# Optimization experiments

Hardware: AMD Instinct MI355X
Metric: run time of the kernel (lower is better)

Reference implementation:

```python
import jax, jax.numpy as jnp
import numpy as np

NUM_BASES = 8
DEGREE = 3
KSIZE = 3
DOMAIN = (0.0, 1.0)


def bspline_basis(x, degree, knots):
    """Cox-de Boor recursion, vectorized over all elements of x.
    x: [...] float; knots: [num_bases + degree + 1].
    Returns basis values of shape [..., num_bases].
    (The original torch code evaluates this same recursion per-tap inside
    nested loops; here it is evaluated once, batched, with correct knot
    index bookkeeping. Uniform distinct knots -> no zero denominators.)
    """
    xe = x[..., None]  # [..., 1]
    # degree-0: indicator of each knot interval -> [..., L-1]
    B = ((knots[:-1] <= xe) & (xe < knots[1:])).astype(x.dtype)
    for d in range(1, degree + 1):
        left = (xe - knots[:-(d + 1)]) / (knots[d:-1] - knots[:-(d + 1)]) * B[..., :-1]
        right = (knots[d + 1:] - xe) / (knots[d + 1:] - knots[1:-d]) * B[..., 1:]
        B = left + right  # [..., L-d-1]
    return B  # [..., num_bases]


def setup_inputs() -> dict:
    key = jax.random.key(0)
    k1, k2 = jax.random.split(key)
    # inputs uniform in [0,1) so they lie inside the B-spline domain
    x = jax.random.uniform(k1, (16, 64, 64, 64), dtype=jnp.float32)
    # per-tap spline coefficients: [Cout, Cin, K, K, num_bases]
    coeff = jax.random.normal(k2, (64, 64, KSIZE, KSIZE, NUM_BASES), dtype=jnp.float32)
    return {"x": x, "coeff": coeff}


def reference(x, coeff):
    # normalize to domain (identity for domain=(0,1), kept for faithfulness)
    xn = (x - DOMAIN[0]) / (DOMAIN[1] - DOMAIN[0])
    knots = jnp.linspace(DOMAIN[0], DOMAIN[1], NUM_BASES + DEGREE + 1, dtype=x.dtype)
    # spline basis for every input element: [B, Cin, H, W, nb]
    phi = bspline_basis(xn, DEGREE, knots)
    Bn, Cin, H, W, nb = phi.shape
    Cout = coeff.shape[0]
    # The KAN conv  out[b,o,h,w] = sum_{j,k,l,m} phi[b,j,h+k,w+l,m]*coeff[o,j,k,l,m]
    # is exactly a VALID conv with Cin*nb input channels.
    phi_c = jnp.transpose(phi, (0, 1, 4, 2, 3)).reshape(Bn, Cin * nb, H, W)
    w = jnp.transpose(coeff, (0, 1, 4, 2, 3)).reshape(Cout, Cin * nb, KSIZE, KSIZE)
    out = jax.lax.conv_general_dilated(
        phi_c, w, window_strides=(1, 1), padding="VALID",
        dimension_numbers=("NCHW", "OIHW", "NCHW"))
    return out  # [B, Cout, H-K+1, W-K+1]
```

## Files before the change

kernel.cpp:

```cpp
#include <hip/hip_runtime.h>
#include <hip/hip_bf16.h>


typedef short v8s __attribute__((ext_vector_type(8)));
typedef float v4f __attribute__((ext_vector_type(4)));
typedef unsigned long long u64;
typedef u64 v2u64 __attribute__((ext_vector_type(2)));

#define B_N   16
#define CIN   64
#define COUT  64
#define H_IN  64
#define W_IN  64
#define NB    8
#define HO    62
#define WO    62
#define JC    8
#define NCH   (CIN / JC)
#define ELEMS (3 * JC * W_IN)
#define EPT   (ELEMS / 256)

__device__ __forceinline__ ushort f2bf(float f) {
    uint xu = __float_as_uint(f);
    return (ushort)((xu + 0x7fffu + ((xu >> 16) & 1u)) >> 16);
}

__global__ void prep_coeff_kernel(const float* __restrict__ coeff, ushort* __restrict__ bt) {
    int n = blockIdx.x * 256 + threadIdx.x;
    if (n >= 576 * COUT * NB) return;
    int m = n & 7;
    int o = (n >> 3) & 63;
    int t = n >> 9;
    int j = t / 9;
    int r9 = t - j * 9;
    float v = coeff[(((o * CIN + j) * 9 + r9) << 3) + m];
    bt[n] = f2bf(v);
}

template<bool USE_BT>
__global__ __launch_bounds__(256, 4) void kan_conv_kernel(
        const float* __restrict__ x, const ushort* __restrict__ cb,
        const float* __restrict__ coeff_f, float* __restrict__ out) {
    const int h    = blockIdx.x;
    const int b    = blockIdx.y;
    const int tid  = threadIdx.x;
    const int lane = tid & 63;
    const int wv   = tid >> 6;
    const int g    = lane >> 4;
    const int l15  = lane & 15;
    const int obase = (wv >> 1) << 5;
    const int wbase = (wv & 1) << 5;

    __shared__ __align__(16) ushort phi_lds[3 * JC * W_IN * NB];
    __shared__ uint lut[72];

    if (tid < 72) {
        int tap = tid;
        int j  = tap / 9;
        int r9 = tap - j * 9;
        int kt = r9 / 3;
        int lt = r9 - kt * 3;
        lut[tap] = (uint)(((kt * JC + j) * W_IN) * NB) | ((uint)lt << 16)
                 | ((uint)j << 20) | ((uint)r9 << 24);
    }

    v4f acc00 = {0.f, 0.f, 0.f, 0.f};
    v4f acc01 = acc00, acc10 = acc00, acc11 = acc00;
    const int aoff = obase + l15;

    float xv[EPT];
    #pragma unroll
    for (int it = 0; it < EPT; ++it) {
        int n  = it * 256 + tid;
        int kt = n >> 9;
        int j  = (n >> 6) & (JC - 1);
        int w  = n & (W_IN - 1);
        xv[it] = x[((b * CIN + j) * H_IN + (h + kt)) * W_IN + w];
    }

    for (int jc = 0; jc < NCH; ++jc) {
        #pragma unroll
        for (int it = 0; it < EPT; ++it) {
            int n = it * 256 + tid;
            float s  = xv[it] * 11.0f;
            int i0 = (int)s;
            i0 = i0 < 0 ? 0 : (i0 > 10 ? 10 : i0);
            float u  = s - (float)i0;
            float um = 1.0f - u;
            float u2 = u * u, u3 = u2 * u;
            const float inv6 = 1.0f / 6.0f;
            float n0 = um * um * um * inv6;
            float n1 = (3.0f * u3 - 6.0f * u2 + 4.0f) * inv6;
            float n2 = (-3.0f * u3 + 3.0f * u2 + 3.0f * u + 1.0f) * inv6;
            float n3 = u3 * inv6;
            u64 V = (u64)f2bf(n0) | ((u64)f2bf(n1) << 16)
                  | ((u64)f2bf(n2) << 32) | ((u64)f2bf(n3) << 48);
            int bi = i0 - 3;
            u64 lo = bi < 0 ? (V >> (uint)(-16 * bi))
                   : bi < 4 ? (V << (uint)(16 * bi)) : 0ull;
            u64 hi = bi <= 0 ? 0ull
                   : bi < 4 ? (V >> (uint)(64 - 16 * bi))
                   : (V << (uint)(16 * bi - 64));
            v2u64 pk; pk[0] = lo; pk[1] = hi;
            *reinterpret_cast<v2u64*>(&phi_lds[n << 3]) = pk;
        }
        if (jc + 1 < NCH) {
            int j0n = (jc + 1) * JC;
            #pragma unroll
            for (int it = 0; it < EPT; ++it) {
                int n  = it * 256 + tid;
                int kt = n >> 9;
                int j  = (n >> 6) & (JC - 1);
                int w  = n & (W_IN - 1);
                xv[it] = x[((b * CIN + j0n + j) * H_IN + (h + kt)) * W_IN + w];
            }
        }
        __syncthreads();
        const int t0 = jc * JC * 9;
        const v8s* cbv = USE_BT ? reinterpret_cast<const v8s*>(cb) : nullptr;
        #pragma unroll 6
        for (int kk = 0; kk < (JC * 9 * NB) / 32; ++kk) {
            int tap = (kk << 2) + g;
            uint e = lut[tap];
            int philoc = (int)(e & 0xffffu);
            int lt     = (int)((e >> 16) & 3u);
            int w0 = wbase + l15 + lt;
            int w1 = w0 + 16;
            w0 = w0 < 63 ? w0 : 63;
            w1 = w1 < 63 ? w1 : 63;
            v8s pb0 = *reinterpret_cast<const v8s*>(&phi_lds[philoc + (w0 << 3)]);
            v8s pb1 = *reinterpret_cast<const v8s*>(&phi_lds[philoc + (w1 << 3)]);
            v8s pa0, pa1;
            if constexpr (USE_BT) {
                const v8s* pa = cbv + ((t0 + tap) << 6) + aoff;
                pa0 = pa[0];
                pa1 = pa[16];
            } else {
                int j  = (int)((e >> 20) & 15u);
                int r9 = (int)((e >> 24) & 15u);
                const float* cf = coeff_f + (((aoff * CIN + (jc * JC + j)) * 9 + r9) << 3);
                #pragma unroll
                for (int z = 0; z < 8; ++z) pa0[z] = (short)f2bf(cf[z]);
                const float* cf2 = cf + (CIN * 9 * NB * 16);
                #pragma unroll
                for (int z = 0; z < 8; ++z) pa1[z] = (short)f2bf(cf2[z]);
            }
            acc00 = __builtin_amdgcn_mfma_f32_16x16x32_bf16(pa0, pb0, acc00, 0, 0, 0);
            acc01 = __builtin_amdgcn_mfma_f32_16x16x32_bf16(pa0, pb1, acc01, 0, 0, 0);
            acc10 = __builtin_amdgcn_mfma_f32_16x16x32_bf16(pa1, pb0, acc10, 0, 0, 0);
            acc11 = __builtin_amdgcn_mfma_f32_16x16x32_bf16(pa1, pb1, acc11, 0, 0, 0);
        }
        __syncthreads();
    }

    const int wc0 = wbase + l15;
    const int wc1 = wc0 + 16;
    #pragma unroll
    for (int i = 0; i < 2; ++i) {
        v4f a0 = (i == 0) ? acc00 : acc10;
        v4f a1 = (i == 0) ? acc01 : acc11;
        int o = obase + i * 16 + (g << 2);
        #pragma unroll
        for (int r = 0; r < 4; ++r) {
            int off = ((b * COUT + o + r) * HO + h) * WO;
            if (wc0 < WO) out[off + wc0] = a0[r];
            if (wc1 < WO) out[off + wc1] = a1[r];
        }
    }
}

extern "C" void kernel_launch(void* const* d_in, const int* in_sizes, int n_in,
                              void* d_out, int out_size, void* d_ws, size_t ws_size,
                              hipStream_t stream) {
    const float* x     = (const float*)d_in[0];
    const float* coeff = (const float*)d_in[1];
    float* out = (float*)d_out;

    const size_t bt_bytes = (size_t)576 * COUT * NB * 2;
    bool use_bt = ws_size >= bt_bytes;

    if (use_bt) {
        ushort* bt = (ushort*)d_ws;
        prep_coeff_kernel<<<(576 * COUT * NB + 255) / 256, 256, 0, stream>>>(coeff, bt);
        kan_conv_kernel<true><<<dim3(HO, B_N), 256, 0, stream>>>(x, bt, coeff, out);
    } else {
        kan_conv_kernel<false><<<dim3(HO, B_N), 256, 0, stream>>>(x, nullptr, coeff, out);
    }
}
```

Baseline: 59.32 us.

## Compute two output rows per block and reuse coefficient fragments across rows

Each block now produces two adjacent output rows from four loaded input rows instead of one row from three. Every coefficient fragment loaded for kernel row r feeds both output rows, so weight traffic per output falls and input rows are shared across the pair. Each wave now covers all 64 output channels for a 16-wide column strip. The phi LDS layout is padded with a row stride of 520 to ease bank conflicts. The cost is more accumulator registers, a drop in launch bounds occupancy from 4 to 2 blocks, and half as many blocks in the grid.

After: 75.69 us. 27.6% more time.

```diff
diff --git a/kernel.cpp b/kernel.cpp
--- a/kernel.cpp
+++ b/kernel.cpp
@@ -17,7 +17,10 @@
 #define WO    62
 #define JC    8
 #define NCH   (CIN / JC)
-#define ELEMS (3 * JC * W_IN)
+#define NROWS 4
+#define ROWSTRIDE 520
+#define RSTRIDE   (JC * ROWSTRIDE)
+#define ELEMS (NROWS * JC * W_IN)
 #define EPT   (ELEMS / 256)
 
 __device__ __forceinline__ ushort f2bf(float f) {
@@ -38,50 +41,56 @@
 }
 
 template<bool USE_BT>
-__global__ __launch_bounds__(256, 4) void kan_conv_kernel(
+__global__ __launch_bounds__(256, 2) void kan_conv_kernel(
         const float* __restrict__ x, const ushort* __restrict__ cb,
         const float* __restrict__ coeff_f, float* __restrict__ out) {
-    const int h    = blockIdx.x;
+    const int h0   = blockIdx.x * 2;
     const int b    = blockIdx.y;
     const int tid  = threadIdx.x;
     const int lane = tid & 63;
-    const int wv   = tid >> 6;
+    const int wq   = tid >> 6;
     const int g    = lane >> 4;
     const int l15  = lane & 15;
-    const int obase = (wv >> 1) << 5;
-    const int wbase = (wv & 1) << 5;
 
-    __shared__ __align__(16) ushort phi_lds[3 * JC * W_IN * NB];
-    __shared__ uint lut[72];
+    __shared__ __align__(16) ushort phi_lds[NROWS * RSTRIDE];
 
-    if (tid < 72) {
-        int tap = tid;
-        int j  = tap / 9;
-        int r9 = tap - j * 9;
-        int kt = r9 / 3;
-        int lt = r9 - kt * 3;
-        lut[tap] = (uint)(((kt * JC + j) * W_IN) * NB) | ((uint)lt << 16)
-                 | ((uint)j << 20) | ((uint)r9 << 24);
+    int baddr[6];
+    int abase[6];
+    #pragma unroll
+    for (int s = 0; s < 6; ++s) {
+        int c   = s * 4 + g;
+        int jl  = c / 3;
+        int lc  = c - jl * 3;
+        int bq  = wq * 16 + l15 + lc;
+        bq = bq < 63 ? bq : 63;
+        baddr[s] = (jl * ROWSTRIDE + bq * NB) * 2;
+        abase[s] = ((jl * 9 + lc) * COUT + l15) * 16;
     }
 
-    v4f acc00 = {0.f, 0.f, 0.f, 0.f};
-    v4f acc01 = acc00, acc10 = acc00, acc11 = acc00;
-    const int aoff = obase + l15;
+    v4f acc0[4], acc1[4];
+    #pragma unroll
+    for (int ot = 0; ot < 4; ++ot) {
+        acc0[ot] = (v4f){0.f, 0.f, 0.f, 0.f};
+        acc1[ot] = (v4f){0.f, 0.f, 0.f, 0.f};
+    }
 
     float xv[EPT];
     #pragma unroll
     for (int it = 0; it < EPT; ++it) {
-        int n  = it * 256 + tid;
-        int kt = n >> 9;
-        int j  = (n >> 6) & (JC - 1);
-        int w  = n & (W_IN - 1);
-        xv[it] = x[((b * CIN + j) * H_IN + (h + kt)) * W_IN + w];
+        int n = it * 256 + tid;
+        int r = n >> 9;
+        int j = (n >> 6) & (JC - 1);
+        int w = n & (W_IN - 1);
+        xv[it] = x[((b * CIN + j) * H_IN + (h0 + r)) * W_IN + w];
     }
 
     for (int jc = 0; jc < NCH; ++jc) {
         #pragma unroll
         for (int it = 0; it < EPT; ++it) {
             int n = it * 256 + tid;
+            int r = n >> 9;
+            int j = (n >> 6) & (JC - 1);
+            int w = n & (W_IN - 1);
             float s  = xv[it] * 11.0f;
             int i0 = (int)s;
             i0 = i0 < 0 ? 0 : (i0 > 10 ? 10 : i0);
@@ -102,69 +111,70 @@
                    : bi < 4 ? (V >> (uint)(64 - 16 * bi))
                    : (V << (uint)(16 * bi - 64));
             v2u64 pk; pk[0] = lo; pk[1] = hi;
-            *reinterpret_cast<v2u64*>(&phi_lds[n << 3]) = pk;
+            *reinterpret_cast<v2u64*>(&phi_lds[(r * JC + j) * ROWSTRIDE + w * NB]) = pk;
         }
         if (jc + 1 < NCH) {
             int j0n = (jc + 1) * JC;
             #pragma unroll
             for (int it = 0; it < EPT; ++it) {
-                int n  = it * 256 + tid;
-                int kt = n >> 9;
-                int j  = (n >> 6) & (JC - 1);
-                int w  = n & (W_IN - 1);
-                xv[it] = x[((b * CIN + j0n + j) * H_IN + (h + kt)) * W_IN + w];
+                int n = it * 256 + tid;
+                int r = n >> 9;
+                int j = (n >> 6) & (JC - 1);
+                int w = n & (W_IN - 1);
+                xv[it] = x[((b * CIN + j0n + j) * H_IN + (h0 + r)) * W_IN + w];
             }
         }
         __syncthreads();
-        const int t0 = jc * JC * 9;
-        const v8s* cbv = USE_BT ? reinterpret_cast<const v8s*>(cb) : nullptr;
-        #pragma unroll 6
-        for (int kk = 0; kk < (JC * 9 * NB) / 32; ++kk) {
-            int tap = (kk << 2) + g;
-            uint e = lut[tap];
-            int philoc = (int)(e & 0xffffu);
-            int lt     = (int)((e >> 16) & 3u);
-            int w0 = wbase + l15 + lt;
-            int w1 = w0 + 16;
-            w0 = w0 < 63 ? w0 : 63;
-            w1 = w1 < 63 ? w1 : 63;
-            v8s pb0 = *reinterpret_cast<const v8s*>(&phi_lds[philoc + (w0 << 3)]);
-            v8s pb1 = *reinterpret_cast<const v8s*>(&phi_lds[philoc + (w1 << 3)]);
-            v8s pa0, pa1;
-            if constexpr (USE_BT) {
-                const v8s* pa = cbv + ((t0 + tap) << 6) + aoff;
-                pa0 = pa[0];
-                pa1 = pa[16];
-            } else {
-                int j  = (int)((e >> 20) & 15u);
-                int r9 = (int)((e >> 24) & 15u);
-                const float* cf = coeff_f + (((aoff * CIN + (jc * JC + j)) * 9 + r9) << 3);
-                #pragma unroll
-                for (int z = 0; z < 8; ++z) pa0[z] = (short)f2bf(cf[z]);
-                const float* cf2 = cf + (CIN * 9 * NB * 16);
-                #pragma unroll
-                for (int z = 0; z < 8; ++z) pa1[z] = (short)f2bf(cf2[z]);
+        const char* cbb  = (const char*)cb + (size_t)(jc * JC * 9) * (COUT * NB * 2);
+        const char* ldsb = (const char*)phi_lds;
+        const int j0 = jc * JC;
+        #pragma unroll
+        for (int s = 0; s < 6; ++s) {
+            v8s ak[3][4];
+            #pragma unroll
+            for (int r = 0; r < NROWS; ++r) {
+                v8s pb = *reinterpret_cast<const v8s*>(ldsb + baddr[s] + r * (RSTRIDE * 2));
+                if (r < 3) {
+                    #pragma unroll
+                    for (int ot = 0; ot < 4; ++ot) {
+                        if constexpr (USE_BT) {
+                            ak[r][ot] = *reinterpret_cast<const v8s*>(
+                                cbb + abase[s] + r * (3 * COUT * NB * 2) + ot * (16 * NB * 2));
+                        } else {
+                            int c  = s * 4 + g;
+                            int jl = c / 3;
+                            int lc = c - jl * 3;
+                            int o  = ot * 16 + l15;
+                            const float* cf = coeff_f +
+                                (((o * CIN + (j0 + jl)) * 9 + (r * 3 + lc)) << 3);
+                            #pragma unroll
+                            for (int z = 0; z < 8; ++z) ak[r][ot][z] = (short)f2bf(cf[z]);
+                        }
+                        acc0[ot] = __builtin_amdgcn_mfma_f32_16x16x32_bf16(ak[r][ot], pb, acc0[ot], 0, 0, 0);
+                    }
+                }
+                if (r >= 1) {
+                    #pragma unroll
+                    for (int ot = 0; ot < 4; ++ot) {
+                        acc1[ot] = __builtin_amdgcn_mfma_f32_16x16x32_bf16(ak[r - 1][ot], pb, acc1[ot], 0, 0, 0);
+                    }
+                }
             }
-            acc00 = __builtin_amdgcn_mfma_f32_16x16x32_bf16(pa0, pb0, acc00, 0, 0, 0);
-            acc01 = __builtin_amdgcn_mfma_f32_16x16x32_bf16(pa0, pb1, acc01, 0, 0, 0);
-            acc10 = __builtin_amdgcn_mfma_f32_16x16x32_bf16(pa1, pb0, acc10, 0, 0, 0);
-            acc11 = __builtin_amdgcn_mfma_f32_16x16x32_bf16(pa1, pb1, acc11, 0, 0, 0);
         }
         __syncthreads();
     }
 
-    const int wc0 = wbase + l15;
-    const int wc1 = wc0 + 16;
-    #pragma unroll
-    for (int i = 0; i < 2; ++i) {
-        v4f a0 = (i == 0) ? acc00 : acc10;
-        v4f a1 = (i == 0) ? acc01 : acc11;
-        int o = obase + i * 16 + (g << 2);
+    const int w = wq * 16 + l15;
+    if (w < WO) {
         #pragma unroll
-        for (int r = 0; r < 4; ++r) {
-            int off = ((b * COUT + o + r) * HO + h) * WO;
-            if (wc0 < WO) out[off + wc0] = a0[r];
-            if (wc1 < WO) out[off + wc1] = a1[r];
+        for (int ot = 0; ot < 4; ++ot) {
+            int o = ot * 16 + (g << 2);
+            #pragma unroll
+            for (int r = 0; r < 4; ++r) {
+                int base = ((b * COUT + o + r) * HO + h0) * WO + w;
+                out[base]      = acc0[ot][r];
+                out[base + WO] = acc1[ot][r];
+            }
         }
     }
 }
@@ -182,8 +192,8 @@
     if (use_bt) {
         ushort* bt = (ushort*)d_ws;
         prep_coeff_kernel<<<(576 * COUT * NB + 255) / 256, 256, 0, stream>>>(coeff, bt);
-        kan_conv_kernel<true><<<dim3(HO, B_N), 256, 0, stream>>>(x, bt, coeff, out);
+        kan_conv_kernel<true><<<dim3(HO / 2, B_N), 256, 0, stream>>>(x, bt, coeff, out);
     } else {
-        kan_conv_kernel<false><<<dim3(HO, B_N), 256, 0, stream>>>(x, nullptr, coeff, out);
+        kan_conv_kernel<false><<<dim3(HO / 2, B_N), 256, 0, stream>>>(x, nullptr, coeff, out);
     }
 }
```

## Compute two output rows per block with register-pipelined spline basis

Applied to the files above, without the earlier changes.

The main kernel now has each block produce two output rows. It loads four input rows of basis values into LDS and reuses each coefficient fragment across both rows, so redundant basis computation and coefficient loads per row are reduced. The basis evaluation for the next channel chunk is interleaved with the MFMA loop in registers, overlapping ALU work with matrix math. The grid is halved, the launch bound drops to 2 blocks per SM and register use rises, which lowers occupancy and parallelism.

New measurement: 69.25 us. 16.7% more time.

```diff
diff --git a/kernel.cpp b/kernel.cpp
--- a/kernel.cpp
+++ b/kernel.cpp
@@ -17,8 +17,6 @@
 #define WO    62
 #define JC    8
 #define NCH   (CIN / JC)
-#define ELEMS (3 * JC * W_IN)
-#define EPT   (ELEMS / 256)
 
 __device__ __forceinline__ ushort f2bf(float f) {
     uint xu = __float_as_uint(f);
@@ -37,10 +35,156 @@
     bt[n] = f2bf(v);
 }
 
-template<bool USE_BT>
-__global__ __launch_bounds__(256, 4) void kan_conv_kernel(
+#define MFMA(a, b, c) __builtin_amdgcn_mfma_f32_16x16x32_bf16((a), (b), (c), 0, 0, 0)
+
+__global__ __launch_bounds__(256, 2) void kan_conv_hp(
         const float* __restrict__ x, const ushort* __restrict__ cb,
-        const float* __restrict__ coeff_f, float* __restrict__ out) {
+        float* __restrict__ out) {
+    const int h0   = blockIdx.x * 2;
+    const int b    = blockIdx.y;
+    const int tid  = threadIdx.x;
+    const int lane = tid & 63;
+    const int wv   = tid >> 6;
+    const int oh   = wv >> 1;
+    const int wh   = wv & 1;
+    const int g    = lane >> 4;
+    const int l15  = lane & 15;
+
+    __shared__ __align__(16) ushort phi_lds[4 * JC * W_IN * NB];
+
+    int baddr0[6], baddr1[6], abase[6];
+    #pragma unroll
+    for (int s = 0; s < 6; ++s) {
+        int c  = s * 4 + g;
+        int jl = c / 3;
+        int lc = c - jl * 3;
+        int w0 = wh * 32 + l15 + lc;
+        int w1 = w0 + 16; w1 = w1 < 63 ? w1 : 63;
+        baddr0[s] = jl * 1024 + w0 * 16;
+        baddr1[s] = jl * 1024 + w1 * 16;
+        abase[s]  = ((jl * 9 + lc) * COUT + oh * 32 + l15) * 16;
+    }
+
+    v4f acc[2][2][2];
+    #pragma unroll
+    for (int h = 0; h < 2; ++h)
+        #pragma unroll
+        for (int ot = 0; ot < 2; ++ot)
+            #pragma unroll
+            for (int wf = 0; wf < 2; ++wf)
+                acc[h][ot][wf] = (v4f){0.f, 0.f, 0.f, 0.f};
+
+    float xreg[8];
+    v2u64 phiv[8];
+
+    auto xload = [&](int jcn) {
+        int j0n = jcn * JC;
+        #pragma unroll
+        for (int it = 0; it < 8; ++it) {
+            int n = it * 256 + tid;
+            xreg[it] = x[((b * CIN + j0n + ((n >> 6) & 7)) * H_IN
+                          + (h0 + (n >> 9))) * W_IN + (n & 63)];
+        }
+    };
+    auto phiE = [&](int e) {
+        float s_ = xreg[e] * 11.0f;
+        int i0 = (int)s_;
+        i0 = i0 < 0 ? 0 : (i0 > 10 ? 10 : i0);
+        float u  = s_ - (float)i0;
+        float um = 1.0f - u;
+        float u2 = u * u, u3 = u2 * u;
+        const float inv6 = 1.0f / 6.0f;
+        float n0 = um * um * um * inv6;
+        float n1 = (3.0f * u3 - 6.0f * u2 + 4.0f) * inv6;
+        float n2 = (-3.0f * u3 + 3.0f * u2 + 3.0f * u + 1.0f) * inv6;
+        float n3 = u3 * inv6;
+        u64 V = (u64)f2bf(n0) | ((u64)f2bf(n1) << 16)
+              | ((u64)f2bf(n2) << 32) | ((u64)f2bf(n3) << 48);
+        int bi = i0 - 3;
+        u64 lo = bi < 0 ? (V >> (uint)(-16 * bi))
+               : bi < 4 ? (V << (uint)(16 * bi)) : 0ull;
+        u64 hi = bi <= 0 ? 0ull
+               : bi < 4 ? (V >> (uint)(64 - 16 * bi))
+               : (V << (uint)(16 * bi - 64));
+        phiv[e][0] = lo; phiv[e][1] = hi;
+    };
+
+    xload(0);
+    #pragma unroll
+    for (int e = 0; e < 8; ++e) phiE(e);
+
+    for (int jc = 0; jc < NCH; ++jc) {
+        __syncthreads();
+        #pragma unroll
+        for (int it = 0; it < 8; ++it)
+            *reinterpret_cast<v2u64*>(&phi_lds[(it * 256 + tid) << 3]) = phiv[it];
+        if (jc + 1 < NCH) xload(jc + 1);
+        __syncthreads();
+        const char* bb  = (const char*)phi_lds;
+        const char* cbb = (const char*)cb + (size_t)jc * (72 * COUT * NB * 2);
+        #pragma unroll
+        for (int s = 0; s < 6; ++s) {
+            v8s pb0 = *reinterpret_cast<const v8s*>(bb + baddr0[s]);
+            v8s pb1 = *reinterpret_cast<const v8s*>(bb + baddr1[s]);
+            v8s a00 = *reinterpret_cast<const v8s*>(cbb + abase[s]);
+            v8s a01 = *reinterpret_cast<const v8s*>(cbb + abase[s] + 256);
+            acc[0][0][0] = MFMA(a00, pb0, acc[0][0][0]);
+            acc[0][0][1] = MFMA(a00, pb1, acc[0][0][1]);
+            acc[0][1][0] = MFMA(a01, pb0, acc[0][1][0]);
+            acc[0][1][1] = MFMA(a01, pb1, acc[0][1][1]);
+            pb0 = *reinterpret_cast<const v8s*>(bb + 8192 + baddr0[s]);
+            pb1 = *reinterpret_cast<const v8s*>(bb + 8192 + baddr1[s]);
+            v8s a10 = *reinterpret_cast<const v8s*>(cbb + abase[s] + 3072);
+            v8s a11 = *reinterpret_cast<const v8s*>(cbb + abase[s] + 3072 + 256);
+            acc[0][0][0] = MFMA(a10, pb0, acc[0][0][0]);
+            acc[0][0][1] = MFMA(a10, pb1, acc[0][0][1]);
+            acc[0][1][0] = MFMA(a11, pb0, acc[0][1][0]);
+            acc[0][1][1] = MFMA(a11, pb1, acc[0][1][1]);
+            acc[1][0][0] = MFMA(a00, pb0, acc[1][0][0]);
+            acc[1][0][1] = MFMA(a00, pb1, acc[1][0][1]);
+            acc[1][1][0] = MFMA(a01, pb0, acc[1][1][0]);
+            acc[1][1][1] = MFMA(a01, pb1, acc[1][1][1]);
+            pb0 = *reinterpret_cast<const v8s*>(bb + 16384 + baddr0[s]);
+            pb1 = *reinterpret_cast<const v8s*>(bb + 16384 + baddr1[s]);
+            v8s a20 = *reinterpret_cast<const v8s*>(cbb + abase[s] + 6144);
+            v8s a21 = *reinterpret_cast<const v8s*>(cbb + abase[s] + 6144 + 256);
+            acc[0][0][0] = MFMA(a20, pb0, acc[0][0][0]);
+            acc[0][0][1] = MFMA(a20, pb1, acc[0][0][1]);
+            acc[0][1][0] = MFMA(a21, pb0, acc[0][1][0]);
+            acc[0][1][1] = MFMA(a21, pb1, acc[0][1][1]);
+            acc[1][0][0] = MFMA(a10, pb0, acc[1][0][0]);
+            acc[1][0][1] = MFMA(a10, pb1, acc[1][0][1]);
+            acc[1][1][0] = MFMA(a11, pb0, acc[1][1][0]);
+            acc[1][1][1] = MFMA(a11, pb1, acc[1][1][1]);
+            pb0 = *reinterpret_cast<const v8s*>(bb + 24576 + baddr0[s]);
+            pb1 = *reinterpret_cast<const v8s*>(bb + 24576 + baddr1[s]);
+            acc[1][0][0] = MFMA(a20, pb0, acc[1][0][0]);
+            acc[1][0][1] = MFMA(a20, pb1, acc[1][0][1]);
+            acc[1][1][0] = MFMA(a21, pb0, acc[1][1][0]);
+            acc[1][1][1] = MFMA(a21, pb1, acc[1][1][1]);
+            if (s < 4 && jc + 1 < NCH) { phiE(2 * s); phiE(2 * s + 1); }
+        }
+    }
+
+    const int w0c = wh * 32 + l15;
+    const int w1c = w0c + 16;
+    #pragma unroll
+    for (int h = 0; h < 2; ++h)
+        #pragma unroll
+        for (int ot = 0; ot < 2; ++ot) {
+            int o = oh * 32 + ot * 16 + (g << 2);
+            #pragma unroll
+            for (int r = 0; r < 4; ++r) {
+                int base = ((b * COUT + o + r) * HO + (h0 + h)) * WO;
+                if (w0c < WO) out[base + w0c] = acc[h][ot][0][r];
+                if (w1c < WO) out[base + w1c] = acc[h][ot][1][r];
+            }
+        }
+}
+
+__global__ __launch_bounds__(256, 4) void kan_conv_fb(
+        const float* __restrict__ x, const float* __restrict__ coeff_f,
+        float* __restrict__ out) {
     const int h    = blockIdx.x;
     const int b    = blockIdx.y;
     const int tid  = threadIdx.x;
@@ -53,7 +197,6 @@
 
     __shared__ __align__(16) ushort phi_lds[3 * JC * W_IN * NB];
     __shared__ uint lut[72];
-
     if (tid < 72) {
         int tap = tid;
         int j  = tap / 9;
@@ -63,24 +206,18 @@
         lut[tap] = (uint)(((kt * JC + j) * W_IN) * NB) | ((uint)lt << 16)
                  | ((uint)j << 20) | ((uint)r9 << 24);
     }
-
     v4f acc00 = {0.f, 0.f, 0.f, 0.f};
     v4f acc01 = acc00, acc10 = acc00, acc11 = acc00;
     const int aoff = obase + l15;
-
-    float xv[EPT];
-    #pragma unroll
-    for (int it = 0; it < EPT; ++it) {
-        int n  = it * 256 + tid;
-        int kt = n >> 9;
-        int j  = (n >> 6) & (JC - 1);
-        int w  = n & (W_IN - 1);
-        xv[it] = x[((b * CIN + j) * H_IN + (h + kt)) * W_IN + w];
-    }
-
+    float xv[6];
+    #pragma unroll
+    for (int it = 0; it < 6; ++it) {
+        int n = it * 256 + tid;
+        xv[it] = x[((b * CIN + ((n >> 6) & 7)) * H_IN + (h + (n >> 9))) * W_IN + (n & 63)];
+    }
     for (int jc = 0; jc < NCH; ++jc) {
         #pragma unroll
-        for (int it = 0; it < EPT; ++it) {
+        for (int it = 0; it < 6; ++it) {
             int n = it * 256 + tid;
             float s  = xv[it] * 11.0f;
             int i0 = (int)s;
@@ -107,19 +244,15 @@
         if (jc + 1 < NCH) {
             int j0n = (jc + 1) * JC;
             #pragma unroll
-            for (int it = 0; it < EPT; ++it) {
-                int n  = it * 256 + tid;
-                int kt = n >> 9;
-                int j  = (n >> 6) & (JC - 1);
-                int w  = n & (W_IN - 1);
-                xv[it] = x[((b * CIN + j0n + j) * H_IN + (h + kt)) * W_IN + w];
+            for (int it = 0; it < 6; ++it) {
+                int n = it * 256 + tid;
+                xv[it] = x[((b * CIN + j0n + ((n >> 6) & 7)) * H_IN + (h + (n >> 9))) * W_IN + (n & 63)];
             }
         }
         __syncthreads();
-        const int t0 = jc * JC * 9;
-        const v8s* cbv = USE_BT ? reinterpret_cast<const v8s*>(cb) : nullptr;
+        const int j0 = jc * JC;
         #pragma unroll 6
-        for (int kk = 0; kk < (JC * 9 * NB) / 32; ++kk) {
+        for (int kk = 0; kk < 18; ++kk) {
             int tap = (kk << 2) + g;
             uint e = lut[tap];
             int philoc = (int)(e & 0xffffu);
@@ -130,29 +263,22 @@
             w1 = w1 < 63 ? w1 : 63;
             v8s pb0 = *reinterpret_cast<const v8s*>(&phi_lds[philoc + (w0 << 3)]);
             v8s pb1 = *reinterpret_cast<const v8s*>(&phi_lds[philoc + (w1 << 3)]);
+            int j  = (int)((e >> 20) & 15u);
+            int r9 = (int)((e >> 24) & 15u);
+            const float* cf = coeff_f + (((aoff * CIN + (j0 + j)) * 9 + r9) << 3);
             v8s pa0, pa1;
-            if constexpr (USE_BT) {
-                const v8s* pa = cbv + ((t0 + tap) << 6) + aoff;
-                pa0 = pa[0];
-                pa1 = pa[16];
-            } else {
-                int j  = (int)((e >> 20) & 15u);
-                int r9 = (int)((e >> 24) & 15u);
-                const float* cf = coeff_f + (((aoff * CIN + (jc * JC + j)) * 9 + r9) << 3);
-                #pragma unroll
-                for (int z = 0; z < 8; ++z) pa0[z] = (short)f2bf(cf[z]);
-                const float* cf2 = cf + (CIN * 9 * NB * 16);
-                #pragma unroll
-                for (int z = 0; z < 8; ++z) pa1[z] = (short)f2bf(cf2[z]);
-            }
-            acc00 = __builtin_amdgcn_mfma_f32_16x16x32_bf16(pa0, pb0, acc00, 0, 0, 0);
-            acc01 = __builtin_amdgcn_mfma_f32_16x16x32_bf16(pa0, pb1, acc01, 0, 0, 0);
-            acc10 = __builtin_amdgcn_mfma_f32_16x16x32_bf16(pa1, pb0, acc10, 0, 0, 0);
-            acc11 = __builtin_amdgcn_mfma_f32_16x16x32_bf16(pa1, pb1, acc11, 0, 0, 0);
+            #pragma unroll
+            for (int z = 0; z < 8; ++z) pa0[z] = (short)f2bf(cf[z]);
+            const float* cf2 = cf + (CIN * 9 * NB * 16);
+            #pragma unroll
+            for (int z = 0; z < 8; ++z) pa1[z] = (short)f2bf(cf2[z]);
+            acc00 = MFMA(pa0, pb0, acc00);
+            acc01 = MFMA(pa0, pb1, acc01);
+            acc10 = MFMA(pa1, pb0, acc10);
+            acc11 = MFMA(pa1, pb1, acc11);
         }
         __syncthreads();
     }
-
     const int wc0 = wbase + l15;
     const int wc1 = wc0 + 16;
     #pragma unroll
@@ -177,13 +303,11 @@
     float* out = (float*)d_out;
 
     const size_t bt_bytes = (size_t)576 * COUT * NB * 2;
-    bool use_bt = ws_size >= bt_bytes;
-
-    if (use_bt) {
+    if (ws_size >= bt_bytes) {
         ushort* bt = (ushort*)d_ws;
         prep_coeff_kernel<<<(576 * COUT * NB + 255) / 256, 256, 0, stream>>>(coeff, bt);
-        kan_conv_kernel<true><<<dim3(HO, B_N), 256, 0, stream>>>(x, bt, coeff, out);
+        kan_conv_hp<<<dim3(HO / 2, B_N), 256, 0, stream>>>(x, bt, out);
     } else {
-        kan_conv_kernel<false><<<dim3(HO, B_N), 256, 0, stream>>>(x, nullptr, coeff, out);
-    }
-}
+        kan_conv_fb<<<dim3(HO, B_N), 256, 0, stream>>>(x, coeff, out);
+    }
+}
```
